# Kernel optimization log

Measured on AMD Instinct MI355X. Metric: run time of the kernel, lower is better.

## Reference

```python
import jax, jax.numpy as jnp
import numpy as np

TEMPERATURE = 0.5
B, D = 4096, 256


def setup_inputs() -> dict:
    key = jax.random.key(0)
    k1, k2 = jax.random.split(key)
    z_i = jax.random.normal(k1, (B, D), dtype=jnp.float32)
    z_j = jax.random.normal(k2, (B, D), dtype=jnp.float32)
    return {"z_i": z_i, "z_j": z_j}


def reference(z_i, z_j):
    batch = z_i.shape[0]
    n = 2 * batch
    z = jnp.concatenate([z_i, z_j], axis=0)                      # [2B, D]
    z = z / jnp.linalg.norm(z, axis=1, keepdims=True)            # L2-normalize rows
    # cosine_similarity of unit vectors == dot product -> single GEMM
    sim = jnp.einsum('id,jd->ij', z, z) / TEMPERATURE            # [2B, 2B]
    mask = jnp.eye(n, dtype=bool)
    sim = jnp.where(mask, -jnp.inf, sim)                         # mask self-similarity
    positives = jnp.concatenate(
        [jnp.diagonal(sim, offset=batch), jnp.diagonal(sim, offset=-batch)], axis=0
    )                                                            # [2B]
    loss = -positives + jax.nn.logsumexp(sim, axis=1)            # [2B]
    return loss.mean()
```

## Files before the change

kernel.cpp:

```cpp
#include <hip/hip_runtime.h>
#include <hip/hip_bf16.h>
#include <stdint.h>
#include <stddef.h>


#define B_ROWS 4096
#define D_DIM  256
#define N_ROWS 8192
#define BM 128
#define BN 64

typedef __bf16 bf16;
typedef bf16  bf16x8  __attribute__((ext_vector_type(8)));
typedef bf16  bf16x4  __attribute__((ext_vector_type(4)));
typedef float floatx4 __attribute__((ext_vector_type(4)));

__global__ __launch_bounds__(256) void normalize_kernel(
    const float* __restrict__ z_i, const float* __restrict__ z_j,
    bf16* __restrict__ zn, float* __restrict__ sumexp) {
  const int wave = threadIdx.x >> 6;
  const int lane = threadIdx.x & 63;
  const int row  = blockIdx.x * 4 + wave;
  const float* src = (row < B_ROWS) ? (z_i + (size_t)row * D_DIM)
                                    : (z_j + (size_t)(row - B_ROWS) * D_DIM);
  float4 v = ((const float4*)src)[lane];
  float ss = v.x * v.x + v.y * v.y + v.z * v.z + v.w * v.w;
  #pragma unroll
  for (int m = 1; m < 64; m <<= 1) ss += __shfl_xor(ss, m);
  const float rn = rsqrtf(ss);
  bf16x4 o;
  o[0] = (bf16)(v.x * rn);
  o[1] = (bf16)(v.y * rn);
  o[2] = (bf16)(v.z * rn);
  o[3] = (bf16)(v.w * rn);
  ((bf16x4*)(zn + (size_t)row * D_DIM))[lane] = o;
  if (lane == 0) sumexp[row] = 0.f;
}

__global__ __launch_bounds__(256, 2) void simexp_kernel(
    const bf16* __restrict__ zn, float* __restrict__ sumexp,
    float* __restrict__ pos) {
  const int tid   = threadIdx.x;
  const int wave  = tid >> 6;
  const int lane  = tid & 63;
  const int lcol  = lane & 15;
  const int lquad = lane >> 4;
  const int wr = (wave >> 1) * 64;
  const int wc = (wave & 1) * 32;
  const int ri = blockIdx.x >> 3;
  const int cj = blockIdx.x & 7;
  const int row_base = ri * BM;
  const int niter = (cj == 7 && ri < 32) ? 10 : 8;

  auto jt64 = [&](int it) {
    return 2 * ((ri + 4 * cj + (it >> 1)) & 63) + (it & 1);
  };

  floatx4 af[4][8];
  #pragma unroll
  for (int ti = 0; ti < 4; ++ti) {
    const bf16* arow =
        zn + (size_t)(row_base + wr + ti * 16 + lcol) * D_DIM + lquad * 8;
    #pragma unroll
    for (int kq = 0; kq < 8; ++kq)
      af[ti][kq] = *(const floatx4*)(arow + kq * 32);
  }

  float rowsum[4][4];
  #pragma unroll
  for (int ti = 0; ti < 4; ++ti)
    #pragma unroll
    for (int r = 0; r < 4; ++r) rowsum[ti][r] = 0.f;

  const int boff0 = (wc + 0 * 16 + lcol) * D_DIM + lquad * 8;
  const int boff1 = (wc + 1 * 16 + lcol) * D_DIM + lquad * 8;

  #pragma unroll 1
  for (int t = 0; t < niter; ++t) {
    const int jt = jt64(t);
    const bf16* bbase = zn + (size_t)jt * BN * D_DIM;

    floatx4 acc[4][2];
    #pragma unroll
    for (int ti = 0; ti < 4; ++ti)
      #pragma unroll
      for (int tj = 0; tj < 2; ++tj) acc[ti][tj] = floatx4{0.f, 0.f, 0.f, 0.f};

    #pragma unroll
    for (int kq = 0; kq < 8; ++kq) {
      bf16x8 bfr[2];
      bfr[0] = *(const bf16x8*)(bbase + boff0 + kq * 32);
      bfr[1] = *(const bf16x8*)(bbase + boff1 + kq * 32);
      #pragma unroll
      for (int ti = 0; ti < 4; ++ti)
        #pragma unroll
        for (int tj = 0; tj < 2; ++tj)
          acc[ti][tj] = __builtin_amdgcn_mfma_f32_16x16x32_bf16(
              __builtin_bit_cast(bf16x8, af[ti][kq]), bfr[tj], acc[ti][tj],
              0, 0, 0);
    }

    const int s    = 4 * cj + (t >> 1);
    const bool diag = (s == 0);
    const bool posT = (s == 32);
    const int col_base = jt * BN;
    float colsum[2] = {0.f, 0.f};
    #pragma unroll
    for (int ti = 0; ti < 4; ++ti) {
      #pragma unroll
      for (int tj = 0; tj < 2; ++tj) {
        #pragma unroll
        for (int r = 0; r < 4; ++r) {
          const float v = acc[ti][tj][r];
          float e = __builtin_amdgcn_exp2f(v * 2.8853900817779268f);
          if (diag || posT) {
            const int rg = row_base + wr + ti * 16 + lquad * 4 + r;
            const int cg = col_base + wc + tj * 16 + lcol;
            if (diag && cg == rg) e = 0.f;
            if (posT && cg == rg + B_ROWS) {
              pos[rg] = 2.0f * v;
              pos[cg] = 2.0f * v;
            }
          }
          rowsum[ti][r] += e;
          colsum[tj]    += e;
        }
      }
    }

    if (!diag) {
      #pragma unroll
      for (int tj = 0; tj < 2; ++tj) {
        float cs = colsum[tj];
        cs += __shfl_xor(cs, 16);
        cs += __shfl_xor(cs, 32);
        if (lquad == 0)
          atomicAdd(&sumexp[col_base + wc + tj * 16 + lcol], cs);
      }
    }
  }

  #pragma unroll
  for (int ti = 0; ti < 4; ++ti) {
    #pragma unroll
    for (int r = 0; r < 4; ++r) {
      float s2 = rowsum[ti][r];
      s2 += __shfl_xor(s2, 1);
      s2 += __shfl_xor(s2, 2);
      s2 += __shfl_xor(s2, 4);
      s2 += __shfl_xor(s2, 8);
      if (lcol == 0) {
        const int grow = row_base + wr + ti * 16 + lquad * 4 + r;
        atomicAdd(&sumexp[grow], s2);
      }
    }
  }
}

__global__ __launch_bounds__(1024) void reduce_kernel(
    const float* __restrict__ sumexp, const float* __restrict__ pos,
    float* __restrict__ out) {
  __shared__ float ws[16];
  const int tid = threadIdx.x;
  float s = 0.f;
  const float ln2 = 0.6931471805599453f;
  for (int k = tid; k < N_ROWS; k += 1024)
    s += __builtin_amdgcn_logf(sumexp[k]) * ln2 - pos[k];
  #pragma unroll
  for (int m = 1; m < 64; m <<= 1) s += __shfl_xor(s, m);
  const int wave = tid >> 6, lane = tid & 63;
  if (lane == 0) ws[wave] = s;
  __syncthreads();
  if (wave == 0) {
    float t = (lane < 16) ? ws[lane] : 0.f;
    #pragma unroll
    for (int m = 1; m < 16; m <<= 1) t += __shfl_xor(t, m);
    if (lane == 0) out[0] = t * (1.0f / N_ROWS);
  }
}

extern "C" void kernel_launch(void* const* d_in, const int* in_sizes, int n_in,
                              void* d_out, int out_size, void* d_ws,
                              size_t ws_size, hipStream_t stream) {
  const float* z_i = (const float*)d_in[0];
  const float* z_j = (const float*)d_in[1];
  float* out = (float*)d_out;

  bf16* zn = (bf16*)d_ws;
  float* sumexp = (float*)((char*)d_ws + (size_t)N_ROWS * D_DIM * sizeof(bf16));
  float* pos = sumexp + N_ROWS;

  normalize_kernel<<<N_ROWS / 4, 256, 0, stream>>>(z_i, z_j, zn, sumexp);
  simexp_kernel<<<512, 256, 0, stream>>>(zn, sumexp, pos);
  reduce_kernel<<<1, 1024, 0, stream>>>(sumexp, pos, out);
}
```

Measured before the change: 111.7 us.

## Stage A tile in swizzled LDS, shrink row tile to 64, double grid

The row tile shrinks from 128 to 64 rows and the grid doubles to 1024 blocks. Each block now loads its A tile into LDS through global_load_lds with an XOR swizzle, instead of keeping A fragments in registers. All four waves share the same 64 A rows, and each wave covers a different 32-column slice of a 64-column B tile. This frees registers so the launch bound can target four blocks per SIMD for more occupancy and parallelism. The cost is extra LDS reads per MFMA, a block-wide barrier, and tail handling that lets only half the waves do the positive-pair tile.

```diff
diff --git a/kernel.cpp b/kernel.cpp
--- a/kernel.cpp
+++ b/kernel.cpp
@@ -7,8 +7,7 @@
 #define B_ROWS 4096
 #define D_DIM  256
 #define N_ROWS 8192
-#define BM 128
-#define BN 64
+#define BM 64
 
 typedef __bf16 bf16;
 typedef bf16  bf16x8  __attribute__((ext_vector_type(8)));
@@ -37,33 +36,36 @@
   if (lane == 0) sumexp[row] = 0.f;
 }
 
-__global__ __launch_bounds__(256, 2) void simexp_kernel(
+__global__ __launch_bounds__(256, 4) void simexp_kernel(
     const bf16* __restrict__ zn, float* __restrict__ sumexp,
     float* __restrict__ pos) {
+  __shared__ __align__(16) bf16 As[BM * D_DIM];
+
   const int tid   = threadIdx.x;
   const int wave  = tid >> 6;
   const int lane  = tid & 63;
   const int lcol  = lane & 15;
   const int lquad = lane >> 4;
-  const int wr = (wave >> 1) * 64;
-  const int wc = (wave & 1) * 32;
   const int ri = blockIdx.x >> 3;
   const int cj = blockIdx.x & 7;
   const int row_base = ri * BM;
-  const int niter = (cj == 7 && ri < 32) ? 10 : 8;
-
-  auto jt64 = [&](int it) {
-    return 2 * ((ri + 4 * cj + (it >> 1)) & 63) + (it & 1);
-  };
-
-  floatx4 af[4][8];
-  #pragma unroll
-  for (int ti = 0; ti < 4; ++ti) {
-    const bf16* arow =
-        zn + (size_t)(row_base + wr + ti * 16 + lcol) * D_DIM + lquad * 8;
-    #pragma unroll
-    for (int kq = 0; kq < 8; ++kq)
-      af[ti][kq] = *(const floatx4*)(arow + kq * 32);
+  const bool tail_block = (cj == 7 && ri < 64);
+  const int niter = tail_block ? 5 : 4;
+
+  {
+    const bf16* asrc = zn + (size_t)row_base * D_DIM;
+    #pragma unroll
+    for (int it = 0; it < 8; ++it) {
+      const int s   = it * 256 + tid;
+      const int n   = s >> 5;
+      const int kcs = s & 31;
+      const int kc  = (kcs & 24) | ((kcs & 7) ^ (n & 7));
+      __builtin_amdgcn_global_load_lds(
+          (const __attribute__((address_space(1))) unsigned int*)
+              (asrc + (size_t)n * D_DIM + kc * 8),
+          (__attribute__((address_space(3))) unsigned int*)&As[s * 8],
+          16, 0, 0);
+    }
   }
 
   float rowsum[4][4];
@@ -72,13 +74,19 @@
     #pragma unroll
     for (int r = 0; r < 4; ++r) rowsum[ti][r] = 0.f;
 
-  const int boff0 = (wc + 0 * 16 + lcol) * D_DIM + lquad * 8;
-  const int boff1 = (wc + 1 * 16 + lcol) * D_DIM + lquad * 8;
+  const int slice_col = (wave & 1) * 32;
+  const int boff0 = (slice_col + lcol) * D_DIM + lquad * 8;
+  const int boff1 = (slice_col + 16 + lcol) * D_DIM + lquad * 8;
+
+  __syncthreads();
 
   #pragma unroll 1
-  for (int t = 0; t < niter; ++t) {
-    const int jt = jt64(t);
-    const bf16* bbase = zn + (size_t)jt * BN * D_DIM;
+  for (int q = 0; q < niter; ++q) {
+    const bool tail = (q == 4);
+    if (tail && wave >= 2) break;
+    const int ct = tail ? (ri + 64)
+                        : ((ri + 8 * cj + 2 * q + (wave >> 1)) & 127);
+    const bf16* bbase = zn + (size_t)ct * BM * D_DIM;
 
     floatx4 acc[4][2];
     #pragma unroll
@@ -88,22 +96,23 @@
 
     #pragma unroll
     for (int kq = 0; kq < 8; ++kq) {
-      bf16x8 bfr[2];
-      bfr[0] = *(const bf16x8*)(bbase + boff0 + kq * 32);
-      bfr[1] = *(const bf16x8*)(bbase + boff1 + kq * 32);
-      #pragma unroll
-      for (int ti = 0; ti < 4; ++ti)
-        #pragma unroll
-        for (int tj = 0; tj < 2; ++tj)
-          acc[ti][tj] = __builtin_amdgcn_mfma_f32_16x16x32_bf16(
-              __builtin_bit_cast(bf16x8, af[ti][kq]), bfr[tj], acc[ti][tj],
-              0, 0, 0);
-    }
-
-    const int s    = 4 * cj + (t >> 1);
-    const bool diag = (s == 0);
-    const bool posT = (s == 32);
-    const int col_base = jt * BN;
+      const int kc   = kq * 4 + lquad;
+      const int slot = (kc & 24) | ((kc & 7) ^ (lcol & 7));
+      const bf16x8 b0 = *(const bf16x8*)(bbase + boff0 + kq * 32);
+      const bf16x8 b1 = *(const bf16x8*)(bbase + boff1 + kq * 32);
+      #pragma unroll
+      for (int ti = 0; ti < 4; ++ti) {
+        const bf16x8 a =
+            *(const bf16x8*)&As[(ti * 16 + lcol) * D_DIM + slot * 8];
+        acc[ti][0] = __builtin_amdgcn_mfma_f32_16x16x32_bf16(a, b0, acc[ti][0],
+                                                             0, 0, 0);
+        acc[ti][1] = __builtin_amdgcn_mfma_f32_16x16x32_bf16(a, b1, acc[ti][1],
+                                                             0, 0, 0);
+      }
+    }
+
+    const bool diagw = (cj == 0 && q == 0 && wave < 2);
+    const int col_base = ct * BM + slice_col;
     float colsum[2] = {0.f, 0.f};
     #pragma unroll
     for (int ti = 0; ti < 4; ++ti) {
@@ -113,11 +122,11 @@
         for (int r = 0; r < 4; ++r) {
           const float v = acc[ti][tj][r];
           float e = __builtin_amdgcn_exp2f(v * 2.8853900817779268f);
-          if (diag || posT) {
-            const int rg = row_base + wr + ti * 16 + lquad * 4 + r;
-            const int cg = col_base + wc + tj * 16 + lcol;
-            if (diag && cg == rg) e = 0.f;
-            if (posT && cg == rg + B_ROWS) {
+          if (diagw || tail) {
+            const int rg = row_base + ti * 16 + lquad * 4 + r;
+            const int cg = col_base + tj * 16 + lcol;
+            if (diagw && cg == rg) e = 0.f;
+            if (tail && cg == rg + B_ROWS) {
               pos[rg] = 2.0f * v;
               pos[cg] = 2.0f * v;
             }
@@ -128,14 +137,14 @@
       }
     }
 
-    if (!diag) {
+    if (!diagw) {
       #pragma unroll
       for (int tj = 0; tj < 2; ++tj) {
         float cs = colsum[tj];
         cs += __shfl_xor(cs, 16);
         cs += __shfl_xor(cs, 32);
         if (lquad == 0)
-          atomicAdd(&sumexp[col_base + wc + tj * 16 + lcol], cs);
+          atomicAdd(&sumexp[col_base + tj * 16 + lcol], cs);
       }
     }
   }
@@ -150,7 +159,7 @@
       s2 += __shfl_xor(s2, 4);
       s2 += __shfl_xor(s2, 8);
       if (lcol == 0) {
-        const int grow = row_base + wr + ti * 16 + lquad * 4 + r;
+        const int grow = row_base + ti * 16 + lquad * 4 + r;
         atomicAdd(&sumexp[grow], s2);
       }
     }
@@ -191,6 +200,6 @@
   float* pos = sumexp + N_ROWS;
 
   normalize_kernel<<<N_ROWS / 4, 256, 0, stream>>>(z_i, z_j, zn, sumexp);
-  simexp_kernel<<<512, 256, 0, stream>>>(zn, sumexp, pos);
+  simexp_kernel<<<1024, 256, 0, stream>>>(zn, sumexp, pos);
   reduce_kernel<<<1, 1024, 0, stream>>>(sumexp, pos, out);
 }
```

After: 107.1 us. 4.1% less time.
